# Kernel optimization log

Hardware: AMD Instinct MI355X
Metric: run time of the kernel (lower is better)

## Reference

```python
import jax, jax.numpy as jnp
import numpy as np

LAMBDA_WEIGHT = 1.0


def _soft_argmax(logits):
    # differentiable_argmax: sum_c softmax(logits)[c] * c along class dim
    nc = logits.shape[1]
    probs = jax.nn.softmax(logits, axis=1)
    idx = jnp.arange(nc, dtype=logits.dtype)[None, :, None, None]
    return jnp.sum(probs * idx, axis=1)  # [B, H, W]


def _pair_loss(mask, d):
    # mask: [L] bool over row-major flattened HxW; d: [L] float (col - row).
    # torch.where returns row-major order, coord[:,1]-coord[:,0] == d at masked
    # pixels; second diff is |d_i - d_prev| over consecutive masked pixels.
    L = mask.shape[0]
    pos = jnp.where(mask, jnp.arange(L), -1)
    last = jax.lax.cummax(pos, axis=0)                 # last masked index <= i
    prev = jnp.concatenate([jnp.full((1,), -1), last[:-1]])  # strictly before i
    valid = mask & (prev >= 0)
    dprev = d[jnp.clip(prev, 0, L - 1)]
    s = jnp.sum(jnp.where(valid, jnp.abs(d - dprev), 0.0))
    npairs = jnp.sum(valid)
    npts = jnp.sum(mask)
    mean = s / jnp.maximum(npairs, 1).astype(d.dtype)
    # N==0 contributes 0 (the `continue`); N==1 gives an empty-mean (NaN) in
    # torch -- guarded to 0 here (such degenerate classes are skipped).
    return jnp.where(npts >= 2, mean / (npts + 1).astype(d.dtype), 0.0)


def reference(logits, labels):
    bs, nc, h, w = logits.shape
    seg = jnp.floor(jax.lax.stop_gradient(_soft_argmax(logits))).astype(jnp.int32)
    seg = seg.reshape(bs, h * w)                       # [B, L] row-major
    # d[i] = col - row for flattened index i
    i = jnp.arange(h * w)
    d = ((i % w) - (i // w)).astype(jnp.float32)       # [L]
    classes = jnp.arange(1, nc, dtype=jnp.int32)       # skip background c=0
    masks = seg[:, None, :] == classes[None, :, None]  # [B, nc-1, L]
    per = jax.vmap(jax.vmap(_pair_loss, in_axes=(0, None)), in_axes=(0, None))(masks, d)
    return jnp.sum(per) * LAMBDA_WEIGHT


def setup_inputs() -> dict:
    key = jax.random.key(0)
    k1, k2 = jax.random.split(key)
    logits = jax.random.normal(k1, (16, 7, 368, 640), dtype=jnp.float32)
    labels = jax.random.randint(k2, (16, 368, 640), 0, 7, dtype=jnp.int64)
    return {"logits": logits, "labels": labels}
```

## Files before the change

### kernel.cpp

```cpp
#include <hip/hip_runtime.h>
#include <cstdint>
#include <cstddef>

#define BB 16
#define CC 7
#define HH 368
#define WW 640
#define LL (HH * WW)
#define NCLS 6
#define NCOMBO (BB * NCLS)
#define SEGW_PB (LL / 4)
#define ROWW (WW / 4)
#define NROWS (BB * HH)
#define BPB (LL / 1024)

__global__ __launch_bounds__(256) void seg_kernel(const float* __restrict__ logits,
                                                  uint32_t* __restrict__ segw) {
    int blk = blockIdx.x;
    int b   = blk / BPB;
    int bb  = blk - b * BPB;
    int t   = threadIdx.x;
    int px  = bb * 1024 + t * 4;
    const float* base = logits + (size_t)b * CC * LL + px;

    float x[CC][4];
#pragma unroll
    for (int c = 0; c < CC; ++c) {
        float4 v = *reinterpret_cast<const float4*>(base + (size_t)c * LL);
        x[c][0] = v.x; x[c][1] = v.y; x[c][2] = v.z; x[c][3] = v.w;
    }

    uint32_t packed = 0;
#pragma unroll
    for (int k = 0; k < 4; ++k) {
        float s = 0.0f, w = 0.0f;
#pragma unroll
        for (int c = 0; c < CC; ++c) {
            float e = __expf(x[c][k]);
            s += e;
            w += e * (float)c;
        }
        int sv = (int)floorf(__fdividef(w, s));
        packed |= (uint32_t)sv << (8 * k);
    }
    segw[(size_t)b * SEGW_PB + bb * 256 + t] = packed;
}

__global__ __launch_bounds__(256) void row_kernel(const uint32_t* __restrict__ segw,
                                                  int4* __restrict__ rowStats) {
    int t    = threadIdx.x;
    int w    = t >> 6;
    int lane = t & 63;
    int grow = blockIdx.x * 4 + w;
    int b = grow / HH;
    int r = grow - b * HH;
    const uint32_t* wp = segw + (size_t)b * SEGW_PB + r * ROWW;

    uint32_t wv[3];
    int      wi[3];
    wi[0] = lane;        wv[0] = wp[lane];
    wi[1] = 64 + lane;   wv[1] = wp[64 + lane];
    wi[2] = 128 + lane;  wv[2] = (lane < 32) ? wp[128 + lane] : 0xFFFFFFFFu;

    int cnt[NCLS], mn[NCLS], mx[NCLS];
#pragma unroll
    for (int c = 0; c < NCLS; ++c) { cnt[c] = 0; mn[c] = 1 << 30; mx[c] = -1; }

#pragma unroll
    for (int q = 0; q < 3; ++q) {
        int colbase = wi[q] << 2;
#pragma unroll
        for (int j = 0; j < 4; ++j) {
            int sv  = (int)((wv[q] >> (8 * j)) & 0xFFu);
            int col = colbase + j;
#pragma unroll
            for (int c = 0; c < NCLS; ++c) {
                int m = (sv == c + 1);
                cnt[c] += m;
                mn[c] = m ? min(mn[c], col) : mn[c];
                mx[c] = m ? max(mx[c], col) : mx[c];
            }
        }
    }

#pragma unroll
    for (int c = 0; c < NCLS; ++c) {
#pragma unroll
        for (int off = 1; off < 64; off <<= 1) {
            cnt[c] += __shfl_down(cnt[c], off, 64);
            mn[c]  = min(mn[c], __shfl_down(mn[c], off, 64));
            mx[c]  = max(mx[c], __shfl_down(mx[c], off, 64));
        }
    }

    if (lane == 0) {
#pragma unroll
        for (int c = 0; c < NCLS; ++c)
            rowStats[(size_t)(b * NCLS + c) * HH + r] = make_int4(cnt[c], mn[c], mx[c], 0);
    }
}

struct St { int S, cnt, first, last; };

__device__ inline St comb(const St& a, const St& b) {
    St r;
    int both = (a.cnt > 0) & (b.cnt > 0);
    r.S     = a.S + b.S + (both ? abs(b.first - a.last) : 0);
    r.cnt   = a.cnt + b.cnt;
    r.first = (a.cnt > 0) ? a.first : b.first;
    r.last  = (b.cnt > 0) ? b.last : a.last;
    return r;
}

__device__ inline St shfl_down_st(const St& s, int off) {
    St r;
    r.S     = __shfl_down(s.S, off, 64);
    r.cnt   = __shfl_down(s.cnt, off, 64);
    r.first = __shfl_down(s.first, off, 64);
    r.last  = __shfl_down(s.last, off, 64);
    return r;
}

__global__ __launch_bounds__(256) void combine_kernel(const int4* __restrict__ rowStats,
                                                      float* __restrict__ out) {
    int combo = blockIdx.x;
    int t = threadIdx.x;
    const int4* rp = rowStats + (size_t)combo * HH;

    St st{0, 0, 0, 0};
    if (t < HH / 2) {
#pragma unroll
        for (int q = 0; q < 2; ++q) {
            int row = 2 * t + q;
            int4 v = rp[row];
            if (v.x > 0) {
                St rs{v.z - v.y, v.x, v.y - row, v.z - row};
                st = comb(st, rs);
            }
        }
    }

#pragma unroll
    for (int off = 1; off < 64; off <<= 1) {
        St o = shfl_down_st(st, off);
        st = comb(st, o);
    }

    __shared__ int4 ws[4];
    int wave = t >> 6;
    if ((t & 63) == 0) ws[wave] = make_int4(st.S, st.cnt, st.first, st.last);
    __syncthreads();

    if (t == 0) {
        St acc{ws[0].x, ws[0].y, ws[0].z, ws[0].w};
#pragma unroll
        for (int q = 1; q < 4; ++q) {
            St o{ws[q].x, ws[q].y, ws[q].z, ws[q].w};
            acc = comb(acc, o);
        }
        int n = acc.cnt;
        if (n >= 2) {
            double res = ((double)acc.S / (double)(n - 1)) / (double)(n + 1);
            atomicAdd(out, (float)res);
        }
    }
}

extern "C" void kernel_launch(void* const* d_in, const int* in_sizes, int n_in,
                              void* d_out, int out_size, void* d_ws, size_t ws_size,
                              hipStream_t stream) {
    const float* logits = (const float*)d_in[0];
    float* out = (float*)d_out;

    uint32_t* segw     = (uint32_t*)d_ws;
    int4*     rowStats = (int4*)((char*)d_ws + (size_t)BB * SEGW_PB * 4);

    hipMemsetAsync(out, 0, sizeof(float) * out_size, stream);
    seg_kernel<<<BB * BPB, 256, 0, stream>>>(logits, segw);
    row_kernel<<<NROWS / 4, 256, 0, stream>>>(segw, rowStats);
    combine_kernel<<<NCOMBO, 256, 0, stream>>>(rowStats, out);
}
```

Measured before the change: 173.3 us.

## Fuse soft-argmax segmentation into per-row stats kernel with nontemporal loads

Merges the segmentation kernel and the row statistics kernel into one, so each wave reads a row of logits for all 7 channels, computes the soft-argmax class in registers, and reduces per-class count/min/max directly. This removes the packed segmentation intermediate write/read and one kernel launch. Loads use nontemporal hints, and a ballot skips the shuffle reduction for classes absent in a row. Each thread now holds more registers (12 pixels × accumulators), which may reduce occupancy for this memory-bound read of about 105 MB.

```diff
diff --git a/kernel.cpp b/kernel.cpp
--- a/kernel.cpp
+++ b/kernel.cpp
@@ -9,82 +9,69 @@
 #define LL (HH * WW)
 #define NCLS 6
 #define NCOMBO (BB * NCLS)
-#define SEGW_PB (LL / 4)
-#define ROWW (WW / 4)
 #define NROWS (BB * HH)
-#define BPB (LL / 1024)
+#define RPB 4
+#define NBLK (NROWS / RPB)
 
-__global__ __launch_bounds__(256) void seg_kernel(const float* __restrict__ logits,
-                                                  uint32_t* __restrict__ segw) {
-    int blk = blockIdx.x;
-    int b   = blk / BPB;
-    int bb  = blk - b * BPB;
-    int t   = threadIdx.x;
-    int px  = bb * 1024 + t * 4;
-    const float* base = logits + (size_t)b * CC * LL + px;
+typedef float v4f __attribute__((ext_vector_type(4)));
 
-    float x[CC][4];
-#pragma unroll
-    for (int c = 0; c < CC; ++c) {
-        float4 v = *reinterpret_cast<const float4*>(base + (size_t)c * LL);
-        x[c][0] = v.x; x[c][1] = v.y; x[c][2] = v.z; x[c][3] = v.w;
-    }
-
-    uint32_t packed = 0;
-#pragma unroll
-    for (int k = 0; k < 4; ++k) {
-        float s = 0.0f, w = 0.0f;
-#pragma unroll
-        for (int c = 0; c < CC; ++c) {
-            float e = __expf(x[c][k]);
-            s += e;
-            w += e * (float)c;
-        }
-        int sv = (int)floorf(__fdividef(w, s));
-        packed |= (uint32_t)sv << (8 * k);
-    }
-    segw[(size_t)b * SEGW_PB + bb * 256 + t] = packed;
+__device__ inline v4f ntload4(const float* p) {
+    return __builtin_nontemporal_load(reinterpret_cast<const v4f*>(p));
 }
 
-__global__ __launch_bounds__(256) void row_kernel(const uint32_t* __restrict__ segw,
-                                                  int4* __restrict__ rowStats) {
+__global__ __launch_bounds__(256) void rowstat_kernel(const float* __restrict__ logits,
+                                                      int4* __restrict__ rowStats) {
     int t    = threadIdx.x;
     int w    = t >> 6;
     int lane = t & 63;
-    int grow = blockIdx.x * 4 + w;
+    int grow = blockIdx.x * RPB + w;
     int b = grow / HH;
     int r = grow - b * HH;
-    const uint32_t* wp = segw + (size_t)b * SEGW_PB + r * ROWW;
+    const float* rowbase = logits + (size_t)b * CC * LL + (size_t)r * WW;
 
-    uint32_t wv[3];
-    int      wi[3];
-    wi[0] = lane;        wv[0] = wp[lane];
-    wi[1] = 64 + lane;   wv[1] = wp[64 + lane];
-    wi[2] = 128 + lane;  wv[2] = (lane < 32) ? wp[128 + lane] : 0xFFFFFFFFu;
+    float sacc[12], wacc[12];
+#pragma unroll
+    for (int k = 0; k < 12; ++k) { sacc[k] = 0.0f; wacc[k] = 0.0f; }
+
+#pragma unroll
+    for (int c = 0; c < CC; ++c) {
+        const float* p = rowbase + (size_t)c * LL;
+        v4f a = ntload4(p + lane * 4);
+        v4f bq = ntload4(p + 256 + lane * 4);
+        v4f cq = (lane < 32) ? ntload4(p + 512 + lane * 4) : v4f{0, 0, 0, 0};
+        float xv[12] = {a.x, a.y, a.z, a.w, bq.x, bq.y, bq.z, bq.w,
+                        cq.x, cq.y, cq.z, cq.w};
+#pragma unroll
+        for (int k = 0; k < 12; ++k) {
+            float e = __expf(xv[k]);
+            sacc[k] += e;
+            wacc[k] += e * (float)c;
+        }
+    }
 
     int cnt[NCLS], mn[NCLS], mx[NCLS];
 #pragma unroll
     for (int c = 0; c < NCLS; ++c) { cnt[c] = 0; mn[c] = 1 << 30; mx[c] = -1; }
 
 #pragma unroll
-    for (int q = 0; q < 3; ++q) {
-        int colbase = wi[q] << 2;
+    for (int k = 0; k < 12; ++k) {
+        if (k >= 8 && lane >= 32) break;
+        int sv  = (int)floorf(__fdividef(wacc[k], sacc[k]));
+        int col = (k < 4) ? (lane * 4 + k)
+                          : (k < 8) ? (256 + lane * 4 + (k - 4))
+                                    : (512 + lane * 4 + (k - 8));
 #pragma unroll
-        for (int j = 0; j < 4; ++j) {
-            int sv  = (int)((wv[q] >> (8 * j)) & 0xFFu);
-            int col = colbase + j;
-#pragma unroll
-            for (int c = 0; c < NCLS; ++c) {
-                int m = (sv == c + 1);
-                cnt[c] += m;
-                mn[c] = m ? min(mn[c], col) : mn[c];
-                mx[c] = m ? max(mx[c], col) : mx[c];
-            }
+        for (int c = 0; c < NCLS; ++c) {
+            int m = (sv == c + 1);
+            cnt[c] += m;
+            mn[c] = m ? min(mn[c], col) : mn[c];
+            mx[c] = m ? max(mx[c], col) : mx[c];
         }
     }
 
 #pragma unroll
     for (int c = 0; c < NCLS; ++c) {
+        if (__ballot(cnt[c] > 0) == 0ull) { cnt[c] = 0; continue; }
 #pragma unroll
         for (int off = 1; off < 64; off <<= 1) {
             cnt[c] += __shfl_down(cnt[c], off, 64);
@@ -172,11 +159,9 @@
     const float* logits = (const float*)d_in[0];
     float* out = (float*)d_out;
 
-    uint32_t* segw     = (uint32_t*)d_ws;
-    int4*     rowStats = (int4*)((char*)d_ws + (size_t)BB * SEGW_PB * 4);
+    int4* rowStats = (int4*)d_ws;
 
     hipMemsetAsync(out, 0, sizeof(float) * out_size, stream);
-    seg_kernel<<<BB * BPB, 256, 0, stream>>>(logits, segw);
-    row_kernel<<<NROWS / 4, 256, 0, stream>>>(segw, rowStats);
+    rowstat_kernel<<<NBLK, 256, 0, stream>>>(logits, rowStats);
     combine_kernel<<<NCOMBO, 256, 0, stream>>>(rowStats, out);
 }
```

Result: faster. 162.2 us (-6.4%).
